# Optimization experiments

Measured on AMD Instinct MI355X. Metric: run time of the kernel, lower is better.

## Reference

```python
import jax, jax.numpy as jnp
import numpy as np

NUM_HEADS = 12
EPS = 1e-6


def softmax_with_policy(attn, policy, eps=EPS):
    # attn: [B, H, N, N]; policy: [B, N, 1]
    B, H, N, _ = attn.shape
    attn_policy = policy.reshape(B, 1, 1, N)
    eye = jnp.eye(N, dtype=attn_policy.dtype).reshape(1, 1, N, N)
    attn_policy = attn_policy + (1.0 - attn_policy) * eye
    max_att = jnp.max(attn, axis=-1, keepdims=True)
    a = jnp.exp((attn - max_att).astype(jnp.float32)) * attn_policy.astype(jnp.float32)
    a = (a + eps / N) / (jnp.sum(a, axis=-1, keepdims=True) + eps)
    return a.astype(attn.dtype)


def setup_inputs() -> dict:
    key = jax.random.key(0)
    k1, k2, k3 = jax.random.split(key, 3)
    B, N, C = 16, 1024, 768
    x = jax.random.normal(k1, (B, N, C), dtype=jnp.float32)
    policy = jax.random.uniform(k2, (B, N, 1), dtype=jnp.float32)
    w_qkv = jax.random.normal(k3, (3 * C, C), dtype=jnp.float32) * (C ** -0.5)
    w_proj = jax.random.normal(jax.random.fold_in(key, 7), (C, C), dtype=jnp.float32) * (C ** -0.5)
    b_proj = jnp.zeros((C,), dtype=jnp.float32)
    return {"x": x, "policy": policy, "w_qkv": w_qkv, "w_proj": w_proj, "b_proj": b_proj, "sampler": 0}


def reference(x, policy, w_qkv, w_proj, b_proj, sampler):
    B, N, C = x.shape
    H = NUM_HEADS
    hd = C // H
    scale = hd ** -0.5
    qkv = (x @ w_qkv.T).reshape(B, N, 3, H, hd)
    qkv = jnp.transpose(qkv, (2, 0, 3, 1, 4))  # [3, B, H, N, hd]
    q, k, v = qkv[0], qkv[1], qkv[2]
    attn = jnp.einsum('bhnd,bhmd->bhnm', q, k) * scale
    attn = softmax_with_policy(attn, policy)
    out = jnp.einsum('bhnm,bhmd->bhnd', attn, v)
    out = jnp.transpose(out, (0, 2, 1, 3)).reshape(B, N, C)
    return out @ w_proj.T + b_proj
```

## Files before the change

kernel.cpp:

```cpp
#include <hip/hip_runtime.h>


#define NB 16
#define NN 1024
#define NC 768
#define NH 12
#define HD 64
#define NM (NB*NN)
#define QKVC (3*NC)
#define QSCALE 0.18033688011112042f
#define PSTR 68
#define TSTR 264

typedef _Float16 f16;
typedef _Float16 f16x8 __attribute__((ext_vector_type(8)));
typedef _Float16 f16x4 __attribute__((ext_vector_type(4)));
typedef _Float16 f16x2 __attribute__((ext_vector_type(2)));
typedef __fp16 fp16x2 __attribute__((ext_vector_type(2)));
typedef float f32x4 __attribute__((ext_vector_type(4)));

#if __has_builtin(__builtin_amdgcn_exp2f)
#define EXP2(x) __builtin_amdgcn_exp2f(x)
#else
#define EXP2(x) exp2f(x)
#endif

#define MFMA16(a,b,c) __builtin_amdgcn_mfma_f32_16x16x32_f16((a),(b),(c),0,0,0)
#define SCHED_FENCE() __builtin_amdgcn_sched_barrier(0)

__device__ inline f16x8 as_f16x8(uint4 u){
  union { uint4 u; f16x8 h; } v; v.u = u; return v.h;
}

__device__ inline void gl_lds16(const f16* g, f16* l){
  __builtin_amdgcn_global_load_lds(
      (const __attribute__((address_space(1))) void*)g,
      (__attribute__((address_space(3))) void*)l, 16, 0, 0);
}

#define CVT_N1 (NM*NC/4)
#define CVT_N2 (QKVC*NC/4)
#define CVT_N3 (NC*NC/4)
__global__ void cvt_all(const float* __restrict__ x, const float* __restrict__ wq,
                        const float* __restrict__ wp, f16* __restrict__ xh,
                        f16* __restrict__ wqh, f16* __restrict__ wph){
  int i = blockIdx.x*blockDim.x + threadIdx.x;
  const float* in; f16* out; int j;
  if (i < CVT_N1){ in = x; out = xh; j = i; }
  else if (i < CVT_N1 + CVT_N2){ in = wq; out = wqh; j = i - CVT_N1; }
  else { in = wp; out = wph; j = i - CVT_N1 - CVT_N2; }
  float4 v = ((const float4*)in)[j];
  f16x4 h; h[0]=(f16)v.x; h[1]=(f16)v.y; h[2]=(f16)v.z; h[3]=(f16)v.w;
  ((f16x4*)out)[j] = h;
}

#define G_STAGE1(SRC, DSTB, KT, RC0, J)                                       \
  gl_lds16(SRC + (size_t)((RC0) + (J)*64 + (t >> 3))*NC + (KT) + sslot*8,     \
           (DSTB) + (J)*4096 + wv*512);

#define G_STAGE4(SRC, DSTB, KT, RC0)                                          \
  { G_STAGE1(SRC, DSTB, KT, RC0, 0) G_STAGE1(SRC, DSTB, KT, RC0, 1)           \
    G_STAGE1(SRC, DSTB, KT, RC0, 2) G_STAGE1(SRC, DSTB, KT, RC0, 3) }

#define PH_READ_BF(KX)                                                        \
  _Pragma("unroll")                                                           \
  for (int nt = 0; nt < 4; nt++)                                              \
    bf[nt] = as_f16x8(*(const uint4*)(B_ + (wc*64 + nt*16 + lr)*64 + (KX)));

#define PH_READ_AF(M0, KX)                                                    \
  _Pragma("unroll")                                                           \
  for (int mt = 0; mt < 4; mt++)                                              \
    af[mt] = as_f16x8(*(const uint4*)(A_ + (wr*128 + ((M0)+mt)*16 + lr)*64 + (KX)));

#define PH_MFMA(M0)                                                           \
  asm volatile("s_waitcnt lgkmcnt(0)" ::: "memory");                          \
  SCHED_FENCE();                                                              \
  __builtin_amdgcn_s_setprio(1);                                              \
  _Pragma("unroll")                                                           \
  for (int mt = 0; mt < 4; mt++)                                              \
    _Pragma("unroll")                                                         \
    for (int nt = 0; nt < 4; nt++)                                            \
      acc[(M0)+mt][nt] = MFMA16(af[mt], bf[nt], acc[(M0)+mt][nt]);            \
  __builtin_amdgcn_s_setprio(0);                                              \
  SCHED_FENCE();

#define GEMM256_PIPELINE(SRC_A, SRC_B, SA, SB)                                \
  G_STAGE4(SRC_A, (SA), 0, R0);                                               \
  G_STAGE4(SRC_B, (SB), 0, C0);                                               \
  _Pragma("unroll 1")                                                         \
  for (int tt = 0; tt < 12; tt++){                                            \
    const int cur = tt & 1;                                                   \
    const int kn = (tt + 1)*64;                                               \
    const bool st = (tt < 11);                                                \
    asm volatile("s_waitcnt vmcnt(0)" ::: "memory");    \
    SCHED_FENCE();                                                            \
    __builtin_amdgcn_s_barrier();                       \
    SCHED_FENCE();                                                            \
    const f16* A_ = (SA) + (cur ? 16384 : 0);                                 \
    const f16* B_ = (SB) + (cur ? 16384 : 0);                                 \
    f16* An_ = (SA) + (cur ? 0 : 16384);                                      \
    f16* Bn_ = (SB) + (cur ? 0 : 16384);                                      \
    f16x8 af[4], bf[4];                                                       \
                                              \
    PH_READ_BF(kxA0); PH_READ_AF(0, kxA0);                                    \
    SCHED_FENCE();                                                            \
    if (st){ G_STAGE1(SRC_A, An_, kn, R0, 0) G_STAGE1(SRC_A, An_, kn, R0, 1) }\
    SCHED_FENCE();                                                            \
    __builtin_amdgcn_s_barrier();                                             \
    PH_MFMA(0);                                                               \
    __builtin_amdgcn_s_barrier();                                             \
    SCHED_FENCE();                                                            \
                                              \
    PH_READ_AF(4, kxA0);                                                      \
    SCHED_FENCE();                                                            \
    if (st){ G_STAGE1(SRC_A, An_, kn, R0, 2) G_STAGE1(SRC_A, An_, kn, R0, 3) }\
    SCHED_FENCE();                                                            \
    __builtin_amdgcn_s_barrier();                                             \
    PH_MFMA(4);                                                               \
    __builtin_amdgcn_s_barrier();                                             \
    SCHED_FENCE();                                                            \
                                              \
    PH_READ_BF(kxA1); PH_READ_AF(0, kxA1);                                    \
    SCHED_FENCE();                                                            \
    if (st){ G_STAGE1(SRC_B, Bn_, kn, C0, 0) G_STAGE1(SRC_B, Bn_, kn, C0, 1) }\
    SCHED_FENCE();                                                            \
    __builtin_amdgcn_s_barrier();                                             \
    PH_MFMA(0);                                                               \
    __builtin_amdgcn_s_barrier();                                             \
    SCHED_FENCE();                                                            \
                                              \
    PH_READ_AF(4, kxA1);                                                      \
    SCHED_FENCE();                                                            \
    if (st){ G_STAGE1(SRC_B, Bn_, kn, C0, 2) G_STAGE1(SRC_B, Bn_, kn, C0, 3) }\
    SCHED_FENCE();                                                            \
    __builtin_amdgcn_s_barrier();                                             \
    PH_MFMA(4);                                                               \
    __builtin_amdgcn_s_barrier();                                             \
    SCHED_FENCE();                                                            \
  }

#define GEMM256_PREAMBLE(NBX, NWG)                                            \
  const int flat_ = blockIdx.y*(NBX) + blockIdx.x;                            \
  const int wg_ = (flat_ % 8)*((NWG)/8) + flat_/8;                            \
  const int R0 = (wg_/(NBX))*256, C0 = (wg_%(NBX))*256;                       \
  const int t = threadIdx.x;                                                  \
  const int wv = t >> 6, l = t & 63, quad = l >> 4, lr = l & 15;              \
  const int wr = wv >> 2, wc = wv & 3;                                        \
  const int sslot = (t & 7) ^ ((t >> 3) & 7);                                 \
  const int xr = lr & 7;                                                      \
  const int kxA0 = (quad ^ xr)*8;                                             \
  const int kxA1 = ((4 + quad) ^ xr)*8;                                       \
  f32x4 acc[8][4] = {};

__launch_bounds__(512, 2)
__global__ void gemm_qkv(const f16* __restrict__ X, const f16* __restrict__ W,
                         f16* __restrict__ Q, f16* __restrict__ K, f16* __restrict__ VT){
  __shared__ __align__(16) f16 smem[256*TSTR];
  f16* const sAp = smem;
  f16* const sBp = smem + 32768;
  GEMM256_PREAMBLE(9, 576);
  GEMM256_PIPELINE(X, W, sAp, sBp);
  const int type = C0 / NC;
  if (type != 2){
#pragma unroll
    for (int nt = 0; nt < 4; nt++){
      int colg = C0 + wc*64 + nt*16 + lr;
      int rem  = colg - type*NC;
      int hh = rem >> 6, d = rem & 63;
#pragma unroll
      for (int mt = 0; mt < 8; mt++)
#pragma unroll
        for (int i = 0; i < 4; i++){
          int row = R0 + wr*128 + mt*16 + quad*4 + i;
          int bb = row >> 10, np = row & 1023;
          int bh = bb*NH + hh;
          float a = acc[mt][nt][i];
          if (type == 0) Q[(bh << 16) + (np << 6) + d] = (f16)(a * QSCALE);
          else           K[(bh << 16) + (np << 6) + d] = (f16)a;
        }
    }
  } else {
    f16* const sT = smem;
#pragma unroll
    for (int nt = 0; nt < 4; nt++){
      const int col = wc*64 + nt*16 + lr;
#pragma unroll
      for (int mt = 0; mt < 8; mt++){
        const int npl = wr*128 + mt*16 + quad*4;
        f16x2 h0; h0[0] = (f16)acc[mt][nt][0]; h0[1] = (f16)acc[mt][nt][1];
        f16x2 h1; h1[0] = (f16)acc[mt][nt][2]; h1[1] = (f16)acc[mt][nt][3];
        *(f16x2*)&sT[col*TSTR + npl]     = h0;
        *(f16x2*)&sT[col*TSTR + npl + 2] = h1;
      }
    }
    __syncthreads();
    const int c    = t >> 1;
    const int half = t & 1;
    const int cg   = (C0 - 2*NC) + c;
    const int bb   = R0 >> 10;
    const int np0  = (R0 & 1023) + half*128;
    const int hh   = cg >> 6, d = cg & 63;
    const int bh   = bb*NH + hh;
    f16* dst = VT + ((size_t)bh << 16) + (d << 10) + np0;
    const f16* srcl = sT + c*TSTR + half*128;
#pragma unroll
    for (int j = 0; j < 16; j++)
      *(uint4*)(dst + j*8) = *(const uint4*)(srcl + j*8);
  }
}

__global__ void vsum_kernel(const f16* __restrict__ VT, float* __restrict__ vsum){
  int bh = blockIdx.x;
  int t = threadIdx.x;
  int row = t >> 2, part = t & 3;
  const uint4* p = (const uint4*)(VT + ((size_t)bh << 16) + row*NN + part*256);
  float s = 0.f;
#pragma unroll
  for (int i = 0; i < 32; i++){
    f16x8 v = as_f16x8(p[i]);
#pragma unroll
    for (int j = 0; j < 8; j++) s += (float)v[j];
  }
  __shared__ float sR[64][4];
  sR[row][part] = s;
  __syncthreads();
  if (t < 64) vsum[bh*64 + t] = sR[t][0] + sR[t][1] + sR[t][2] + sR[t][3];
}

#define STAGE(BUF, KEY0H)                                                     \
  _Pragma("unroll")                                                           \
  for (int j = 0; j < 2; j++){                                                \
    const int s_  = j*256 + t;                                                \
    const int r_  = s_ >> 3;                                                  \
    const int sl_ = (s_ & 7) ^ (r_ & 7);                                      \
    f16* du_ = (f16*)&sK[BUF][(j*256 + (t & 192))*8];                         \
    f16* dv_ = (f16*)&sVT[BUF][(j*256 + (t & 192))*8];                        \
    gl_lds16(Kg  + (size_t)((KEY0H) + r_)*HD + sl_*8, du_);                   \
    gl_lds16(VTg + (size_t)r_*NN + (KEY0H) + sl_*8,   dv_);                   \
  }

__launch_bounds__(256, 3)
__global__ void attn_kernel(const f16* __restrict__ Q, const f16* __restrict__ K,
                            const f16* __restrict__ VT, const float* __restrict__ policy,
                            const float* __restrict__ vsum, f16* __restrict__ O){
  __shared__ f16 sK[2][4096];
  __shared__ f16 sVT[2][4096];
  __shared__ f16 sP[4][2][16][PSTR];
  __shared__ float sPol[1024];

  const int blk = blockIdx.x;
  const int bh = blk % (NB*NH);
  const int qt = blk / (NB*NH);
  const int b = bh / NH;
  const size_t base = (size_t)bh << 16;

  const int t = threadIdx.x;
  const int w = t >> 6, l = t & 63, quad = l >> 4, lr = l & 15;
  const int q0 = qt*128 + w*32;
  const int qrow = q0 + lr;
  const int h = bh - b*NH;
  const int xr = lr & 7;
  const int kx0 = (quad ^ xr)*8;
  const int kx1 = ((4 + quad) ^ xr)*8;

  *(float4*)&sPol[t*4] = *(const float4*)(policy + b*NN + t*4);

  f16x8 qf[2][2];
#pragma unroll
  for (int tq = 0; tq < 2; tq++)
#pragma unroll
    for (int hf = 0; hf < 2; hf++)
      qf[tq][hf] = as_f16x8(*(const uint4*)(Q + base + (size_t)(q0 + tq*16 + lr)*HD + hf*32 + quad*8));

  float vs[4];
#pragma unroll
  for (int nt = 0; nt < 4; nt++) vs[nt] = vsum[bh*64 + nt*16 + lr];

  f16x8 ones;
#pragma unroll
  for (int j = 0; j < 8; j++) ones[j] = (f16)1.0f;

  float m_run[2] = {-INFINITY, -INFINITY};
  f32x4 acc_l[2] = {};
  f32x4 o[2][4] = {};

  const f16* Kg  = K + base;
  const f16* VTg = VT + base;

  STAGE(0, 0);
  asm volatile("s_waitcnt vmcnt(0) lgkmcnt(0)" ::: "memory");
  SCHED_FENCE();
  __builtin_amdgcn_s_barrier();
  SCHED_FENCE();

#pragma unroll 1
  for (int hs = 0; hs < 16; hs++){
    const int cur = hs & 1;
    const int key0h = hs*64;
    if (hs < 15){
      STAGE(cur^1, key0h + 64);
      asm volatile("s_waitcnt vmcnt(4)" ::: "memory");
    } else {
      asm volatile("s_waitcnt vmcnt(0)" ::: "memory");
    }
    SCHED_FENCE();
    __builtin_amdgcn_s_barrier();
    SCHED_FENCE();

    const f16* sKc = (const f16*)sK[cur];
    const f16* sVc = (const f16*)sVT[cur];

    f32x4 accA[4], accB[4];
#pragma unroll
    for (int ct = 0; ct < 4; ct++){ accA[ct] = (f32x4){0,0,0,0}; accB[ct] = (f32x4){0,0,0,0}; }
    __builtin_amdgcn_s_setprio(1);
#pragma unroll
    for (int ct = 0; ct < 4; ct++){
      const f16* kp = sKc + (ct*16 + lr)*64;
      f16x8 k0 = as_f16x8(*(const uint4*)(kp + kx0));
      f16x8 k1 = as_f16x8(*(const uint4*)(kp + kx1));
      accA[ct] = MFMA16(k0, qf[0][0], accA[ct]);
      accA[ct] = MFMA16(k1, qf[0][1], accA[ct]);
      accB[ct] = MFMA16(k0, qf[1][0], accB[ct]);
      accB[ct] = MFMA16(k1, qf[1][1], accB[ct]);
    }
    __builtin_amdgcn_s_setprio(0);

    {
      float mA = m_run[0], mB = m_run[1];
      const bool diag = (hs == 2*qt + (w >> 1));
      if (!diag){
#pragma unroll
        for (int ct = 0; ct < 4; ct++){
          const int kb = ct*16 + quad*4;
          float4 pol4 = *(const float4*)&sPol[key0h + kb];
          const float* p4 = (const float*)&pol4;
          mA = fmaxf(mA, fmaxf(fmaxf(accA[ct][0], accA[ct][1]), fmaxf(accA[ct][2], accA[ct][3])));
          mB = fmaxf(mB, fmaxf(fmaxf(accB[ct][0], accB[ct][1]), fmaxf(accB[ct][2], accB[ct][3])));
          union { f16x4 v; fp16x2 h[2]; } uA, uB;
          uA.h[0] = __builtin_amdgcn_cvt_pkrtz(EXP2(accA[ct][0])*p4[0], EXP2(accA[ct][1])*p4[1]);
          uA.h[1] = __builtin_amdgcn_cvt_pkrtz(EXP2(accA[ct][2])*p4[2], EXP2(accA[ct][3])*p4[3]);
          uB.h[0] = __builtin_amdgcn_cvt_pkrtz(EXP2(accB[ct][0])*p4[0], EXP2(accB[ct][1])*p4[1]);
          uB.h[1] = __builtin_amdgcn_cvt_pkrtz(EXP2(accB[ct][2])*p4[2], EXP2(accB[ct][3])*p4[3]);
          *(f16x4*)&sP[w][0][lr][kb] = uA.v;
          *(f16x4*)&sP[w][1][lr][kb] = uB.v;
        }
      } else {
#pragma unroll
        for (int ct = 0; ct < 4; ct++){
          const int kb = ct*16 + quad*4;
          float4 pol4 = *(const float4*)&sPol[key0h + kb];
          const float* p4 = (const float*)&pol4;
          float eA[4], eB[4];
#pragma unroll
          for (int i2 = 0; i2 < 4; i2++){
            int kg = key0h + kb + i2;
            float polA = (kg == qrow)      ? 1.0f : p4[i2];
            float polB = (kg == qrow + 16) ? 1.0f : p4[i2];
            mA = fmaxf(mA, accA[ct][i2]); mB = fmaxf(mB, accB[ct][i2]);
            eA[i2] = EXP2(accA[ct][i2]) * polA;
            eB[i2] = EXP2(accB[ct][i2]) * polB;
          }
          union { f16x4 v; fp16x2 h[2]; } uA, uB;
          uA.h[0] = __builtin_amdgcn_cvt_pkrtz(eA[0], eA[1]);
          uA.h[1] = __builtin_amdgcn_cvt_pkrtz(eA[2], eA[3]);
          uB.h[0] = __builtin_amdgcn_cvt_pkrtz(eB[0], eB[1]);
          uB.h[1] = __builtin_amdgcn_cvt_pkrtz(eB[2], eB[3]);
          *(f16x4*)&sP[w][0][lr][kb] = uA.v;
          *(f16x4*)&sP[w][1][lr][kb] = uB.v;
        }
      }
      m_run[0] = mA; m_run[1] = mB;
    }

    __builtin_amdgcn_s_setprio(1);
#pragma unroll
    for (int s8g = 0; s8g < 2; s8g++){
      f16x8 pfA = as_f16x8(*(const uint4*)&sP[w][0][lr][s8g*32 + quad*8]);
      f16x8 pfB = as_f16x8(*(const uint4*)&sP[w][1][lr][s8g*32 + quad*8]);
      acc_l[0] = MFMA16(pfA, ones, acc_l[0]);
      acc_l[1] = MFMA16(pfB, ones, acc_l[1]);
      const int sx = ((s8g*4 + quad) ^ xr)*8;
#pragma unroll
      for (int nt = 0; nt < 4; nt++){
        f16x8 vf = as_f16x8(*(const uint4*)(sVc + (nt*16 + lr)*64 + sx));
        o[0][nt] = MFMA16(pfA, vf, o[0][nt]);
        o[1][nt] = MFMA16(pfB, vf, o[1][nt]);
      }
    }
    __builtin_amdgcn_s_setprio(0);
    SCHED_FENCE();
    __builtin_amdgcn_s_barrier();
    SCHED_FENCE();
  }

#pragma unroll
  for (int tq = 0; tq < 2; tq++){
    float mq = m_run[tq];
    mq = fmaxf(mq, __shfl_xor(mq, 16));
    mq = fmaxf(mq, __shfl_xor(mq, 32));
#pragma unroll
    for (int i = 0; i < 4; i++){
      float mi = __shfl(mq, quad*4 + i);
      float E  = EXP2(mi);
      float li = acc_l[tq][i];
      float inv = 1.0f / (li + 1e-6f*E);
      float ec  = (1e-6f/1024.0f)*E;
      int row = q0 + tq*16 + quad*4 + i;
      f16* op = O + (size_t)(b*NN + row)*NC + h*HD;
#pragma unroll
      for (int nt = 0; nt < 4; nt++)
        op[nt*16 + lr] = (f16)((o[tq][nt][i] + ec*vs[nt]) * inv);
    }
  }
}

__launch_bounds__(512, 2)
__global__ void gemm_proj(const f16* __restrict__ A, const f16* __restrict__ W,
                          const float* __restrict__ bias, float* __restrict__ out){
  __shared__ f16 sA[2*16384];
  __shared__ f16 sB[2*16384];
  GEMM256_PREAMBLE(3, 192);
  GEMM256_PIPELINE(A, W, sA, sB);
#pragma unroll
  for (int nt = 0; nt < 4; nt++){
    int colg = C0 + wc*64 + nt*16 + lr;
    float bv = bias[colg];
#pragma unroll
    for (int mt = 0; mt < 8; mt++)
#pragma unroll
      for (int i = 0; i < 4; i++){
        int row = R0 + wr*128 + mt*16 + quad*4 + i;
        out[(size_t)row*NC + colg] = acc[mt][nt][i] + bv;
      }
  }
}

extern "C" void kernel_launch(void* const* d_in, const int* in_sizes, int n_in,
                              void* d_out, int out_size, void* d_ws, size_t ws_size,
                              hipStream_t stream) {
  const float* x      = (const float*)d_in[0];
  const float* policy = (const float*)d_in[1];
  const float* w_qkv  = (const float*)d_in[2];
  const float* w_proj = (const float*)d_in[3];
  const float* b_proj = (const float*)d_in[4];
  float* out = (float*)d_out;

  f16* x_h     = (f16*)d_ws;
  f16* wqkv_h  = x_h + (size_t)NM*NC;
  f16* wproj_h = wqkv_h + (size_t)QKVC*NC;
  f16* q_h     = wproj_h + (size_t)NC*NC;
  f16* k_h     = q_h + (size_t)NM*NC;
  f16* vt_h    = k_h + (size_t)NM*NC;
  float* vsum_f = (float*)(vt_h + (size_t)NM*NC);
  f16* attn_h  = x_h;

  cvt_all<<<(CVT_N1+CVT_N2+CVT_N3)/256, 256, 0, stream>>>(x, w_qkv, w_proj, x_h, wqkv_h, wproj_h);

  gemm_qkv<<<dim3(QKVC/256, NM/256), 512, 0, stream>>>(x_h, wqkv_h, q_h, k_h, vt_h);

  vsum_kernel<<<dim3(NB*NH), 256, 0, stream>>>(vt_h, vsum_f);

  attn_kernel<<<dim3(NB*NH*(NN/128)), 256, 0, stream>>>(q_h, k_h, vt_h, policy, vsum_f, attn_h);

  gemm_proj<<<dim3(NC/256, NM/256), 512, 0, stream>>>(attn_h, wproj_h, b_proj, out);
}
```

Measured before the change: 320.6 us.

## Rewrite projection GEMM with 128x128 tiles and triple-buffered pipeline

Replaces the 256x256-tile, 512-thread projection GEMM with a 128x128-tile, 256-thread kernel that uses a 3-stage LDS ring of BK=32 slices, loaded directly global-to-LDS and gated by explicit vmcnt waits. The 256x256 tiling produced only 192 workgroups for the 16384x768 output, which underfills the device. The smaller tiles give 768 workgroups at the cost of less data reuse per tile and more global traffic. The new code reads LDS without swizzling, so bank conflicts are a risk.

```diff
diff --git a/kernel.cpp b/kernel.cpp
--- a/kernel.cpp
+++ b/kernel.cpp
@@ -139,7 +139,7 @@
     SCHED_FENCE();                                                            \
   }
 
-#define GEMM256_PREAMBLE(NBX, NWG)                                            \
+#define GEMM256_PREAMBLE(NBX, NWG)                                           \
   const int flat_ = blockIdx.y*(NBX) + blockIdx.x;                            \
   const int wg_ = (flat_ % 8)*((NWG)/8) + flat_/8;                            \
   const int R0 = (wg_/(NBX))*256, C0 = (wg_%(NBX))*256;                       \
@@ -415,22 +415,70 @@
   }
 }
 
-__launch_bounds__(512, 2)
+#define P_STAGE(SRC_A, SRC_B, BUF, BK)                                        \
+  _Pragma("unroll")                                                           \
+  for (int r = 0; r < 2; r++){                                                \
+    int row = r*64 + row0;                                                    \
+    gl_lds16(SRC_A + (size_t)(R0 + row)*NC + (BK) + kc0, sA[BUF] + r*2048 + w*512); \
+    gl_lds16(SRC_B + (size_t)(C0 + row)*NC + (BK) + kc0, sB[BUF] + r*2048 + w*512); \
+  }
+
+__launch_bounds__(256)
 __global__ void gemm_proj(const f16* __restrict__ A, const f16* __restrict__ W,
                           const float* __restrict__ bias, float* __restrict__ out){
-  __shared__ f16 sA[2*16384];
-  __shared__ f16 sB[2*16384];
-  GEMM256_PREAMBLE(3, 192);
-  GEMM256_PIPELINE(A, W, sA, sB);
+  __shared__ f16 sA[3][128*32];
+  __shared__ f16 sB[3][128*32];
+  const int flat = blockIdx.y*6 + blockIdx.x;
+  const int wg = (flat % 8)*96 + flat/8;
+  const int R0 = (wg/6)*128, C0 = (wg%6)*128;
+  const int t = threadIdx.x;
+  const int w = t >> 6, l = t & 63, quad = l >> 4, lr = l & 15;
+  const int wr = w >> 1, wc = w & 1;
+  const int row0 = t >> 2, kc0 = (t & 3)*8;
+  f32x4 acc[4][4] = {};
+  P_STAGE(A, W, 0, 0);
+  P_STAGE(A, W, 1, 32);
+#pragma unroll 1
+  for (int kt = 0; kt < 24; kt++){
+    const int cur = kt % 3;
+    if (kt < 22){
+      P_STAGE(A, W, (kt+2) % 3, (kt+2)*32);
+      asm volatile("s_waitcnt vmcnt(8)" ::: "memory");
+    } else if (kt == 22){
+      asm volatile("s_waitcnt vmcnt(4)" ::: "memory");
+    } else {
+      asm volatile("s_waitcnt vmcnt(0)" ::: "memory");
+    }
+    SCHED_FENCE();
+    __builtin_amdgcn_s_barrier();
+    SCHED_FENCE();
+    f16x8 af[4], bf[4];
+#pragma unroll
+    for (int mt = 0; mt < 4; mt++)
+      af[mt] = as_f16x8(*(const uint4*)(sA[cur] + (wr*64 + mt*16 + lr)*32 + quad*8));
+#pragma unroll
+    for (int nt = 0; nt < 4; nt++)
+      bf[nt] = as_f16x8(*(const uint4*)(sB[cur] + (wc*64 + nt*16 + lr)*32 + quad*8));
+    __builtin_amdgcn_s_setprio(1);
+#pragma unroll
+    for (int mt = 0; mt < 4; mt++)
+#pragma unroll
+      for (int nt = 0; nt < 4; nt++)
+        acc[mt][nt] = MFMA16(af[mt], bf[nt], acc[mt][nt]);
+    __builtin_amdgcn_s_setprio(0);
+    SCHED_FENCE();
+    __builtin_amdgcn_s_barrier();
+    SCHED_FENCE();
+  }
 #pragma unroll
   for (int nt = 0; nt < 4; nt++){
     int colg = C0 + wc*64 + nt*16 + lr;
     float bv = bias[colg];
 #pragma unroll
-    for (int mt = 0; mt < 8; mt++)
+    for (int mt = 0; mt < 4; mt++)
 #pragma unroll
       for (int i = 0; i < 4; i++){
-        int row = R0 + wr*128 + mt*16 + quad*4 + i;
+        int row = R0 + wr*64 + mt*16 + quad*4 + i;
         out[(size_t)row*NC + colg] = acc[mt][nt][i] + bv;
       }
   }
@@ -463,5 +511,5 @@
 
   attn_kernel<<<dim3(NB*NH*(NN/128)), 256, 0, stream>>>(q_h, k_h, vt_h, policy, vsum_f, attn_h);
 
-  gemm_proj<<<dim3(NC/256, NM/256), 512, 0, stream>>>(attn_h, wproj_h, b_proj, out);
-}
+  gemm_proj<<<dim3(NC/128, NM/128), 256, 0, stream>>>(attn_h, wproj_h, b_proj, out);
+}
```

After: 313.9 us. -2.1%, faster.
